# Kernel optimization log

Measured on AMD Instinct MI355X. Metric: run time of the kernel, lower is better.

## Reference

```python
import jax, jax.numpy as jnp
import numpy as np

N_INPUTS = 4
ACTIVE_IDX = 0
HIDDEN = 2048
EPS = 1e-6
ROUTER_INPUT_SCALE = float(HIDDEN ** (-1.0))


def _rms_norm(x, w, eps=EPS):
    var = jnp.mean(jnp.square(x), axis=-1, keepdims=True)
    return x * jax.lax.rsqrt(var + eps) * w


def _modalities(x, w_norm, W_router):
    # tanh(router(norm(x) * hidden_size**-1)) -> [B, S, n]
    r = _rms_norm(x, w_norm) * ROUTER_INPUT_SCALE
    return jnp.tanh(r @ W_router.T)


def setup_inputs() -> dict:
    key = jax.random.key(0)
    k0, k1, k2, k3, k4 = jax.random.split(key, 5)
    B, S = 2, 4096
    return {
        "hidden_states": jax.random.normal(k0, (N_INPUTS, B, S, HIDDEN), jnp.float32),
        "activated": jax.random.normal(k1, (B, S, HIDDEN), jnp.float32),
        "w_norm": jnp.ones((HIDDEN,), jnp.float32),
        "W_router": jax.random.normal(k2, (N_INPUTS, HIDDEN), jnp.float32) * 0.02,
        "W_pred": jax.random.normal(k3, (N_INPUTS * N_INPUTS, N_INPUTS), jnp.float32) * 0.02,
        "W_corr": jax.random.normal(k4, (N_INPUTS, N_INPUTS), jnp.float32) * 0.02,
    }


def reference(hidden_states, activated, w_norm, W_router, W_pred, W_corr):
    n = N_INPUTS
    # ---- predict ----
    active = hidden_states[ACTIVE_IDX]                      # [B,S,H]
    mods = _modalities(active, w_norm, W_router)            # [B,S,n]
    coefs = (mods @ W_pred.T)                               # [B,S,n*n]
    coefs = coefs.reshape(*coefs.shape[:-1], n, n)          # [B,S,n,n]
    coefs = jnp.swapaxes(coefs, -1, -2)                     # transpose last two dims
    stacked = jnp.moveaxis(hidden_states, 0, -1)            # [B,S,H,n]
    preds = jnp.einsum('bshk,bskj->bshj', stacked, coefs) + stacked
    predictions = jnp.moveaxis(preds, -1, 0)                # [n,B,S,H]
    # ---- correct ----
    mods_c = _modalities(activated, w_norm, W_router)       # [B,S,n]
    innovation = activated - predictions[ACTIVE_IDX]        # [B,S,H]
    ccoefs = mods_c @ W_corr.T + 1.0                        # [B,S,n]
    corrected = predictions + innovation[None] * jnp.moveaxis(ccoefs, -1, 0)[..., None]
    return corrected                                        # [n,B,S,H]
```

## Files before the change

kernel.cpp:

```cpp
#include <hip/hip_runtime.h>


constexpr int H = 2048;
constexpr int NCHUNK = 8;
constexpr float EPS = 1e-6f;

typedef float f32x4 __attribute__((ext_vector_type(4)));

__global__ __launch_bounds__(256) void altup_wave(
    const float* __restrict__ hs,
    const float* __restrict__ act,
    const float* __restrict__ w_norm,
    const float* __restrict__ W_router,
    const float* __restrict__ W_pred,
    const float* __restrict__ W_corr,
    float* __restrict__ out,
    long long T)
{
    const int lane = threadIdx.x & 63;
    const int wv   = threadIdx.x >> 6;
    const long long t = (long long)blockIdx.x * 4 + wv;
    if (t >= T) return;
    const long long row = t * (long long)H;
    const long long plane = T * (long long)H;
    const int base = lane * 4;

    float p[10];
#pragma unroll
    for (int i = 0; i < 10; ++i) p[i] = 0.f;

#pragma unroll
    for (int c = 0; c < NCHUNK; ++c) {
        const int off = c * 256 + base;
        const f32x4 xa = *reinterpret_cast<const f32x4*>(hs + row + off);
        const f32x4 xc = *reinterpret_cast<const f32x4*>(act + row + off);
        const f32x4 wn = *reinterpret_cast<const f32x4*>(w_norm + off);
        f32x4 wr[4];
#pragma unroll
        for (int i = 0; i < 4; ++i)
            wr[i] = *reinterpret_cast<const f32x4*>(W_router + i * H + off);
#pragma unroll
        for (int e = 0; e < 4; ++e) {
            p[0] += xa[e] * xa[e];
            p[5] += xc[e] * xc[e];
            const float wa = xa[e] * wn[e];
            const float wc = xc[e] * wn[e];
#pragma unroll
            for (int i = 0; i < 4; ++i) {
                p[1 + i] += wa * wr[i][e];
                p[6 + i] += wc * wr[i][e];
            }
        }
    }

#pragma unroll
    for (int m = 1; m < 64; m <<= 1) {
#pragma unroll
        for (int i = 0; i < 10; ++i) p[i] += __shfl_xor(p[i], m, 64);
    }

    const float ris = 1.0f / (float)H;
    const float inv_a = rsqrtf(p[0] * ris + EPS) * ris;
    const float inv_c = rsqrtf(p[5] * ris + EPS) * ris;
    float mods[4], modsc[4];
#pragma unroll
    for (int i = 0; i < 4; ++i) {
        mods[i]  = tanhf(p[1 + i] * inv_a);
        modsc[i] = tanhf(p[6 + i] * inv_c);
    }
    float coefT[4][4];
#pragma unroll
    for (int j = 0; j < 4; ++j)
#pragma unroll
        for (int k = 0; k < 4; ++k) {
            float s = 0.f;
#pragma unroll
            for (int m = 0; m < 4; ++m) s += mods[m] * W_pred[(j * 4 + k) * 4 + m];
            coefT[k][j] = s;
        }
    float ccoef[4];
#pragma unroll
    for (int j = 0; j < 4; ++j) {
        float s = 1.0f;
#pragma unroll
        for (int m = 0; m < 4; ++m) s += modsc[m] * W_corr[j * 4 + m];
        ccoef[j] = s;
    }

#pragma unroll
    for (int c = 0; c < NCHUNK; ++c) {
        const int off = c * 256 + base;
        const f32x4 x0 = *reinterpret_cast<const f32x4*>(hs + row + off);
        const f32x4 x1 = *reinterpret_cast<const f32x4*>(hs + plane + row + off);
        const f32x4 x2 = *reinterpret_cast<const f32x4*>(hs + 2 * plane + row + off);
        const f32x4 x3 = *reinterpret_cast<const f32x4*>(hs + 3 * plane + row + off);
        const f32x4 xc = *reinterpret_cast<const f32x4*>(act + row + off);
        f32x4 o4[4];
#pragma unroll
        for (int e = 0; e < 4; ++e) {
            const float xk[4] = { x0[e], x1[e], x2[e], x3[e] };
            float pred[4];
#pragma unroll
            for (int j = 0; j < 4; ++j) {
                float s = xk[j];
#pragma unroll
                for (int k = 0; k < 4; ++k) s += xk[k] * coefT[k][j];
                pred[j] = s;
            }
            const float innov = xc[e] - pred[0];
#pragma unroll
            for (int j = 0; j < 4; ++j)
                o4[j][e] = pred[j] + innov * ccoef[j];
        }
#pragma unroll
        for (int j = 0; j < 4; ++j)
            *reinterpret_cast<f32x4*>(out + j * plane + row + off) = o4[j];
    }
}

extern "C" void kernel_launch(void* const* d_in, const int* in_sizes, int n_in,
                              void* d_out, int out_size, void* d_ws, size_t ws_size,
                              hipStream_t stream) {
    const float* hs       = (const float*)d_in[0];
    const float* act      = (const float*)d_in[1];
    const float* w_norm   = (const float*)d_in[2];
    const float* W_router = (const float*)d_in[3];
    const float* W_pred   = (const float*)d_in[4];
    const float* W_corr   = (const float*)d_in[5];
    float* out = (float*)d_out;
    const long long T = (long long)in_sizes[0] / (4LL * H);

    const unsigned grid = (unsigned)((T + 3) / 4);
    altup_wave<<<dim3(grid), dim3(256), 0, stream>>>(
        hs, act, w_norm, W_router, W_pred, W_corr, out, T);
}
```

Before: 139.3 us.

## Keep active and activated rows in registers and prefetch other planes

```diff
diff --git a/kernel.cpp b/kernel.cpp
--- a/kernel.cpp
+++ b/kernel.cpp
@@ -2,12 +2,12 @@
 
 
 constexpr int H = 2048;
-constexpr int NCHUNK = 8;
+constexpr int NC = 8;
 constexpr float EPS = 1e-6f;
 
 typedef float f32x4 __attribute__((ext_vector_type(4)));
 
-__global__ __launch_bounds__(256) void altup_wave(
+__global__ __launch_bounds__(256) void altup_deconvoy(
     const float* __restrict__ hs,
     const float* __restrict__ act,
     const float* __restrict__ w_norm,
@@ -25,31 +25,47 @@
     const long long plane = T * (long long)H;
     const int base = lane * 4;
 
+    const float* p0 = hs + row;
+    const float* p1 = hs + plane + row;
+    const float* p2 = hs + 2 * plane + row;
+    const float* p3 = hs + 3 * plane + row;
+    const float* pc = act + row;
+    float* o0 = out + row;
+    float* o1 = out + plane + row;
+    float* o2 = out + 2 * plane + row;
+    float* o3 = out + 3 * plane + row;
+
+    f32x4 x0[NC], xc[NC];
     float p[10];
 #pragma unroll
     for (int i = 0; i < 10; ++i) p[i] = 0.f;
 
 #pragma unroll
-    for (int c = 0; c < NCHUNK; ++c) {
+    for (int c = 0; c < NC; ++c) {
         const int off = c * 256 + base;
-        const f32x4 xa = *reinterpret_cast<const f32x4*>(hs + row + off);
-        const f32x4 xc = *reinterpret_cast<const f32x4*>(act + row + off);
+        x0[c] = *reinterpret_cast<const f32x4*>(p0 + off);
+        xc[c] = *reinterpret_cast<const f32x4*>(pc + off);
+    }
+#pragma unroll
+    for (int c = 0; c < NC; ++c) {
+        const int off = c * 256 + base;
         const f32x4 wn = *reinterpret_cast<const f32x4*>(w_norm + off);
-        f32x4 wr[4];
-#pragma unroll
-        for (int i = 0; i < 4; ++i)
-            wr[i] = *reinterpret_cast<const f32x4*>(W_router + i * H + off);
 #pragma unroll
         for (int e = 0; e < 4; ++e) {
-            p[0] += xa[e] * xa[e];
-            p[5] += xc[e] * xc[e];
-            const float wa = xa[e] * wn[e];
-            const float wc = xc[e] * wn[e];
+            p[0] += x0[c][e] * x0[c][e];
+            p[5] += xc[c][e] * xc[c][e];
+        }
 #pragma unroll
-            for (int i = 0; i < 4; ++i) {
-                p[1 + i] += wa * wr[i][e];
-                p[6 + i] += wc * wr[i][e];
+        for (int i = 0; i < 4; ++i) {
+            const f32x4 wr = *reinterpret_cast<const f32x4*>(W_router + i * H + off);
+            float da = 0.f, dc = 0.f;
+#pragma unroll
+            for (int e = 0; e < 4; ++e) {
+                const float wre = wn[e] * wr[e];
+                da += x0[c][e] * wre;
+                dc += xc[c][e] * wre;
             }
+            p[1 + i] += da; p[6 + i] += dc;
         }
     }
 
@@ -87,18 +103,25 @@
         ccoef[j] = s;
     }
 
+    f32x4 c1 = *reinterpret_cast<const f32x4*>(p1 + base);
+    f32x4 c2 = *reinterpret_cast<const f32x4*>(p2 + base);
+    f32x4 c3 = *reinterpret_cast<const f32x4*>(p3 + base);
+
 #pragma unroll
-    for (int c = 0; c < NCHUNK; ++c) {
+    for (int c = 0; c < NC; ++c) {
         const int off = c * 256 + base;
-        const f32x4 x0 = *reinterpret_cast<const f32x4*>(hs + row + off);
-        const f32x4 x1 = *reinterpret_cast<const f32x4*>(hs + plane + row + off);
-        const f32x4 x2 = *reinterpret_cast<const f32x4*>(hs + 2 * plane + row + off);
-        const f32x4 x3 = *reinterpret_cast<const f32x4*>(hs + 3 * plane + row + off);
-        const f32x4 xc = *reinterpret_cast<const f32x4*>(act + row + off);
-        f32x4 o4[4];
+        f32x4 n1, n2, n3;
+        if (c + 1 < NC) {
+            const int noff = off + 256;
+            n1 = *reinterpret_cast<const f32x4*>(p1 + noff);
+            n2 = *reinterpret_cast<const f32x4*>(p2 + noff);
+            n3 = *reinterpret_cast<const f32x4*>(p3 + noff);
+        }
+
+        f32x4 r0, r1, r2, r3;
 #pragma unroll
         for (int e = 0; e < 4; ++e) {
-            const float xk[4] = { x0[e], x1[e], x2[e], x3[e] };
+            const float xk[4] = { x0[c][e], c1[e], c2[e], c3[e] };
             float pred[4];
 #pragma unroll
             for (int j = 0; j < 4; ++j) {
@@ -107,14 +130,18 @@
                 for (int k = 0; k < 4; ++k) s += xk[k] * coefT[k][j];
                 pred[j] = s;
             }
-            const float innov = xc[e] - pred[0];
-#pragma unroll
-            for (int j = 0; j < 4; ++j)
-                o4[j][e] = pred[j] + innov * ccoef[j];
+            const float innov = xc[c][e] - pred[0];
+            r0[e] = pred[0] + innov * ccoef[0];
+            r1[e] = pred[1] + innov * ccoef[1];
+            r2[e] = pred[2] + innov * ccoef[2];
+            r3[e] = pred[3] + innov * ccoef[3];
         }
-#pragma unroll
-        for (int j = 0; j < 4; ++j)
-            *reinterpret_cast<f32x4*>(out + j * plane + row + off) = o4[j];
+        *reinterpret_cast<f32x4*>(o0 + off) = r0;
+        *reinterpret_cast<f32x4*>(o1 + off) = r1;
+        *reinterpret_cast<f32x4*>(o2 + off) = r2;
+        *reinterpret_cast<f32x4*>(o3 + off) = r3;
+
+        c1 = n1; c2 = n2; c3 = n3;
     }
 }
 
@@ -131,6 +158,6 @@
     const long long T = (long long)in_sizes[0] / (4LL * H);
 
     const unsigned grid = (unsigned)((T + 3) / 4);
-    altup_wave<<<dim3(grid), dim3(256), 0, stream>>>(
+    altup_deconvoy<<<dim3(grid), dim3(256), 0, stream>>>(
         hs, act, w_norm, W_router, W_pred, W_corr, out, T);
 }
```

After: 127.0 us. 1.1x faster.
